# Kernel tuning notes

Hardware: AMD Instinct MI355X
Metric: run time of the kernel (lower is better)

The kernel has to match this reference:

```python
import jax, jax.numpy as jnp
import numpy as np

N_NODES = 100000
N_EDGES = 1600000
IN_CH, HID_CH, OUT_CH, NCLASS = 128, 256, 256, 40


def gcn_conv(x, edge_index, edge_weight, W, b):
    """PyG GCNConv: h = D^{-1/2} (A + I) D^{-1/2} (x @ W) + b, weighted edges."""
    n = x.shape[0]
    row, col = edge_index[0], edge_index[1]
    loop = jnp.arange(n)
    row = jnp.concatenate([row, loop])
    col = jnp.concatenate([col, loop])
    ew = jnp.concatenate([edge_weight, jnp.ones((n,), x.dtype)])  # self-loop weight 1
    deg = jax.ops.segment_sum(ew, col, num_segments=n)
    dinv = jnp.where(deg > 0, jax.lax.rsqrt(deg), 0.0)
    norm = dinv[row] * ew * dinv[col]            # [E+N]
    h = x @ W                                    # transform before propagate (as PyG)
    msg = h[row] * norm[:, None]                 # gather + scale, [E+N, F]
    out = jax.ops.segment_sum(msg, col, num_segments=n)  # scatter-add
    return out + b


def setup_inputs() -> dict:
    key = jax.random.key(0)
    ks = jax.random.split(key, 9)
    x = jax.random.normal(ks[0], (N_NODES, IN_CH), dtype=jnp.float32)
    edge_index = jax.random.randint(ks[1], (2, N_EDGES), 0, N_NODES, dtype=jnp.int64)
    edge_attr = jax.random.uniform(ks[2], (N_EDGES,), dtype=jnp.float32)
    s1 = 1.0 / np.sqrt(IN_CH)
    s2 = 1.0 / np.sqrt(HID_CH)
    s3 = 1.0 / np.sqrt(OUT_CH)
    W1 = jax.random.uniform(ks[3], (IN_CH, HID_CH), jnp.float32, -s1, s1)
    b1 = jnp.zeros((HID_CH,), jnp.float32)
    W2 = jax.random.uniform(ks[4], (HID_CH, OUT_CH), jnp.float32, -s2, s2)
    b2 = jnp.zeros((OUT_CH,), jnp.float32)
    fcW = jax.random.uniform(ks[5], (OUT_CH, NCLASS), jnp.float32, -s3, s3)
    fcb = jax.random.uniform(ks[6], (NCLASS,), jnp.float32, -s3, s3)
    return {"x": x, "edge_index": edge_index, "edge_attr": edge_attr,
            "W1": W1, "b1": b1, "W2": W2, "b2": b2, "fcW": fcW, "fcb": fcb}


def reference(x, edge_index, edge_attr, W1, b1, W2, b2, fcW, fcb):
    # eval mode: dropout is identity
    h = jax.nn.relu(gcn_conv(x, edge_index, edge_attr, W1, b1))
    h = jax.nn.relu(gcn_conv(h, edge_index, edge_attr, W2, b2))
    return h @ fcW + fcb
```

## Files before the change

kernel.cpp:

```cpp
#include <hip/hip_runtime.h>

#define NODES 100000
#define EDGES 1600000

typedef __attribute__((ext_vector_type(8))) short short8;
typedef __attribute__((ext_vector_type(4))) float floatx4;
typedef _Float16 h16;
typedef __attribute__((ext_vector_type(2))) _Float16 h16x2;
typedef __attribute__((ext_vector_type(4))) _Float16 h16x4;
typedef __attribute__((ext_vector_type(8))) _Float16 h16x8;

__device__ inline unsigned short bf16_rne(float x) {
    unsigned u = __float_as_uint(x);
    u += 0x7FFF + ((u >> 16) & 1);
    return (unsigned short)(u >> 16);
}

__device__ inline void load_lds16(void* lds, const void* g) {
    __builtin_amdgcn_global_load_lds((const __attribute__((address_space(1))) void*)g,
                                     (__attribute__((address_space(3))) void*)lds, 16, 0, 0);
}

__global__ __launch_bounds__(256) void k_prep(const float* __restrict__ W1,
                                              unsigned short* __restrict__ W1th, unsigned short* __restrict__ W1tl,
                                              const float* __restrict__ W2,
                                              unsigned short* __restrict__ W2th, unsigned short* __restrict__ W2tl,
                                              const float* __restrict__ x, h16* __restrict__ x16,
                                              unsigned long long* __restrict__ packed, int n) {
    int b = blockIdx.x;
    if (b < 384) {
        const float* W = (b < 128) ? W1 : W2;
        unsigned short* Bth = (b < 128) ? W1th : W2th;
        unsigned short* Btl = (b < 128) ? W1tl : W2tl;
        int K = (b < 128) ? 128 : 256;
        int idx = ((b < 128) ? b : (b - 128)) * 256 + threadIdx.x;
        if (idx < K * 256) {
            int k = idx >> 8, nn = idx & 255;
            float v = W[idx];
            unsigned short h = bf16_rne(v);
            unsigned short l = bf16_rne(v - __uint_as_float((unsigned)h << 16));
            Bth[nn * K + k] = h;
            Btl[nn * K + k] = l;
        }
    } else if (b < 775) {
        int i = (b - 384) * 256 + threadIdx.x;
        if (i < n) packed[i] = 0ull;
    } else {
        int i = (b - 775) * 256 + threadIdx.x;
        if (i < n * 32) {
            float4 v = reinterpret_cast<const float4*>(x)[i];
            h16x4 h;
            h.x = (h16)v.x; h.y = (h16)v.y; h.z = (h16)v.z; h.w = (h16)v.w;
            reinterpret_cast<h16x4*>(x16)[i] = h;
        }
    }
}

__global__ __launch_bounds__(256) void k_hist(unsigned long long* __restrict__ packed,
                                              unsigned short* __restrict__ rank,
                                              const int* __restrict__ col,
                                              const float* __restrict__ ew, int e) {
    int i = blockIdx.x * 256 + threadIdx.x;
    if (i < e) {
        int c = col[i];
        unsigned long long v = (1ull << 40) |
            (unsigned long long)__float2uint_rn(ew[i] * 1048576.0f);
        unsigned long long old = atomicAdd(&packed[c], v);
        rank[i] = (unsigned short)(old >> 40);
    }
}

__global__ __launch_bounds__(256) void k_scan1(const unsigned long long* __restrict__ packed,
                                               int* __restrict__ rowptr,
                                               int* __restrict__ partials,
                                               float* __restrict__ dinv, int n) {
    __shared__ int wtot[4];
    const int tid = threadIdx.x, lane = tid & 63, wid = tid >> 6;
    int i = blockIdx.x * 256 + tid;
    int v = 0;
    if (i < n) {
        unsigned long long p = packed[i];
        v = (int)(p >> 40);
        float deg = 1.0f + (float)(p & 0xFFFFFFFFFFull) * (1.0f / 1048576.0f);
        dinv[i] = rsqrtf(deg);
    }
    int incl = v;
#pragma unroll
    for (int off = 1; off < 64; off <<= 1) {
        int t = __shfl_up(incl, off, 64);
        if (lane >= off) incl += t;
    }
    if (lane == 63) wtot[wid] = incl;
    __syncthreads();
    int woff = 0;
    for (int k = 0; k < wid; ++k) woff += wtot[k];
    if (i < n) rowptr[i] = woff + incl - v;
    if (tid == 255) partials[blockIdx.x] = woff + incl;
}

__global__ __launch_bounds__(512) void k_scan2(int* __restrict__ partials, int nb) {
    __shared__ int wtot[8];
    const int tid = threadIdx.x, lane = tid & 63, wid = tid >> 6;
    int v = (tid < nb) ? partials[tid] : 0;
    int incl = v;
#pragma unroll
    for (int off = 1; off < 64; off <<= 1) {
        int t = __shfl_up(incl, off, 64);
        if (lane >= off) incl += t;
    }
    if (lane == 63) wtot[wid] = incl;
    __syncthreads();
    int woff = 0;
    for (int k = 0; k < wid; ++k) woff += wtot[k];
    if (tid < nb) partials[tid] = woff + incl - v;
}

__global__ __launch_bounds__(256) void k_scan3(int* __restrict__ rowptr,
                                               const int* __restrict__ partials, int n) {
    int i = blockIdx.x * 256 + threadIdx.x;
    if (i < n) rowptr[i] += partials[blockIdx.x];
    if (blockIdx.x == 0 && threadIdx.x == 0) rowptr[n] = EDGES;
}

__global__ __launch_bounds__(256) void k_build(const int* __restrict__ rowptr,
                                               const unsigned short* __restrict__ rank,
                                               int2* __restrict__ meta,
                                               const int* __restrict__ row, const int* __restrict__ col,
                                               const float* __restrict__ ew,
                                               const float* __restrict__ dinv, int e) {
    int i = blockIdx.x * 256 + threadIdx.x;
    if (i >= e) return;
    int r = row[i], c = col[i];
    float w = dinv[r] * ew[i] * dinv[c];
    int pos = rowptr[c] + rank[i];
    meta[pos] = make_int2(r, __float_as_int(w));
}

__global__ __launch_bounds__(256) void k_gather_x(unsigned short* __restrict__ Xh,
                                                  unsigned short* __restrict__ Xl,
                                                  const h16* __restrict__ x16,
                                                  const float* __restrict__ dinv,
                                                  const int* __restrict__ rowptr,
                                                  const int2* __restrict__ meta, int n) {
    int node = (blockIdx.x << 2) + (threadIdx.x >> 6);
    if (node >= n) return;
    const int lane = threadIdx.x & 63;
    const int j = lane << 1;
    float di = dinv[node];
    float s = di * di;
    h16x2 xs = *reinterpret_cast<const h16x2*>(x16 + (size_t)node * 128 + j);
    float2 a0 = make_float2((float)xs.x * s, (float)xs.y * s);
    float2 a1 = make_float2(0.f, 0.f);

    int p = rowptr[node];
    const int end = rowptr[node + 1];
    for (; p + 3 < end; p += 4) {
        int2 m0 = meta[p],     m1 = meta[p + 1];
        int2 m2 = meta[p + 2], m3 = meta[p + 3];
        h16x2 h0 = *reinterpret_cast<const h16x2*>(x16 + (size_t)m0.x * 128 + j);
        h16x2 h1 = *reinterpret_cast<const h16x2*>(x16 + (size_t)m1.x * 128 + j);
        h16x2 h2 = *reinterpret_cast<const h16x2*>(x16 + (size_t)m2.x * 128 + j);
        h16x2 h3 = *reinterpret_cast<const h16x2*>(x16 + (size_t)m3.x * 128 + j);
        float w0 = __int_as_float(m0.y), w1 = __int_as_float(m1.y);
        float w2 = __int_as_float(m2.y), w3 = __int_as_float(m3.y);
        a0.x = fmaf((float)h0.x, w0, a0.x); a0.y = fmaf((float)h0.y, w0, a0.y);
        a1.x = fmaf((float)h1.x, w1, a1.x); a1.y = fmaf((float)h1.y, w1, a1.y);
        a0.x = fmaf((float)h2.x, w2, a0.x); a0.y = fmaf((float)h2.y, w2, a0.y);
        a1.x = fmaf((float)h3.x, w3, a1.x); a1.y = fmaf((float)h3.y, w3, a1.y);
    }
    for (; p < end; ++p) {
        int2 m0 = meta[p];
        h16x2 h0 = *reinterpret_cast<const h16x2*>(x16 + (size_t)m0.x * 128 + j);
        float w0 = __int_as_float(m0.y);
        a0.x = fmaf((float)h0.x, w0, a0.x); a0.y = fmaf((float)h0.y, w0, a0.y);
    }
    a0.x += a1.x; a0.y += a1.y;

    ushort2 hh, ll;
    hh.x = bf16_rne(a0.x); ll.x = bf16_rne(a0.x - __uint_as_float((unsigned)hh.x << 16));
    hh.y = bf16_rne(a0.y); ll.y = bf16_rne(a0.y - __uint_as_float((unsigned)hh.y << 16));
    *reinterpret_cast<ushort2*>(Xh + (size_t)node * 128 + j) = hh;
    *reinterpret_cast<ushort2*>(Xl + (size_t)node * 128 + j) = ll;
}

__global__ __launch_bounds__(256) void k_gather(h16* __restrict__ P,
                                                const h16* __restrict__ H,
                                                const float* __restrict__ dinv,
                                                const int* __restrict__ rowptr,
                                                const int2* __restrict__ meta,
                                                const float* __restrict__ bias, int n) {
    int node = (blockIdx.x << 2) + (threadIdx.x >> 6);
    if (node >= n) return;
    const int lane = threadIdx.x & 63;
    const int j = lane << 2;
    float di = dinv[node];
    float s = di * di;
    float4 b = *reinterpret_cast<const float4*>(bias + j);
    h16x4 hv = *reinterpret_cast<const h16x4*>(H + (size_t)node * 256 + j);
    float4 acc;
    acc.x = fmaf((float)hv.x, s, b.x); acc.y = fmaf((float)hv.y, s, b.y);
    acc.z = fmaf((float)hv.z, s, b.z); acc.w = fmaf((float)hv.w, s, b.w);
    float4 acc2 = make_float4(0.f, 0.f, 0.f, 0.f);

    int p = rowptr[node];
    const int end = rowptr[node + 1];
    for (; p + 3 < end; p += 4) {
        int2 m0 = meta[p],     m1 = meta[p + 1];
        int2 m2 = meta[p + 2], m3 = meta[p + 3];
        h16x4 h0 = *reinterpret_cast<const h16x4*>(H + (size_t)m0.x * 256 + j);
        h16x4 h1 = *reinterpret_cast<const h16x4*>(H + (size_t)m1.x * 256 + j);
        h16x4 h2 = *reinterpret_cast<const h16x4*>(H + (size_t)m2.x * 256 + j);
        h16x4 h3 = *reinterpret_cast<const h16x4*>(H + (size_t)m3.x * 256 + j);
        float w0 = __int_as_float(m0.y), w1 = __int_as_float(m1.y);
        float w2 = __int_as_float(m2.y), w3 = __int_as_float(m3.y);
        acc.x  = fmaf((float)h0.x, w0, acc.x);  acc.y  = fmaf((float)h0.y, w0, acc.y);
        acc.z  = fmaf((float)h0.z, w0, acc.z);  acc.w  = fmaf((float)h0.w, w0, acc.w);
        acc2.x = fmaf((float)h1.x, w1, acc2.x); acc2.y = fmaf((float)h1.y, w1, acc2.y);
        acc2.z = fmaf((float)h1.z, w1, acc2.z); acc2.w = fmaf((float)h1.w, w1, acc2.w);
        acc.x  = fmaf((float)h2.x, w2, acc.x);  acc.y  = fmaf((float)h2.y, w2, acc.y);
        acc.z  = fmaf((float)h2.z, w2, acc.z);  acc.w  = fmaf((float)h2.w, w2, acc.w);
        acc2.x = fmaf((float)h3.x, w3, acc2.x); acc2.y = fmaf((float)h3.y, w3, acc2.y);
        acc2.z = fmaf((float)h3.z, w3, acc2.z); acc2.w = fmaf((float)h3.w, w3, acc2.w);
    }
    for (; p < end; ++p) {
        int2 m0 = meta[p];
        h16x4 h0 = *reinterpret_cast<const h16x4*>(H + (size_t)m0.x * 256 + j);
        float w0 = __int_as_float(m0.y);
        acc.x = fmaf((float)h0.x, w0, acc.x); acc.y = fmaf((float)h0.y, w0, acc.y);
        acc.z = fmaf((float)h0.z, w0, acc.z); acc.w = fmaf((float)h0.w, w0, acc.w);
    }
    acc.x += acc2.x; acc.y += acc2.y; acc.z += acc2.z; acc.w += acc2.w;

    h16x4 o;
    o.x = (h16)fmaxf(acc.x, 0.f); o.y = (h16)fmaxf(acc.y, 0.f);
    o.z = (h16)fmaxf(acc.z, 0.f); o.w = (h16)fmaxf(acc.w, 0.f);
    *reinterpret_cast<h16x4*>(P + (size_t)node * 256 + j) = o;
}

template<bool SPLIT>
__global__ __launch_bounds__(256) void k_gemm_bf16(const unsigned short* __restrict__ Ahg,
                                                   const unsigned short* __restrict__ Alg,
                                                   const unsigned short* __restrict__ Bth,
                                                   const unsigned short* __restrict__ Btl,
                                                   h16* __restrict__ Hh,
                                                   unsigned short* __restrict__ Ph,
                                                   unsigned short* __restrict__ Pl,
                                                   const float* __restrict__ bias,
                                                   int M, int K) {
    __shared__ __attribute__((aligned(16))) char ldsAh[8192];
    __shared__ __attribute__((aligned(16))) char ldsAl[8192];
    __shared__ __attribute__((aligned(16))) char ldsBh[8192];
    __shared__ __attribute__((aligned(16))) char ldsBl[8192];
    const int tid = threadIdx.x;
    const int lane = tid & 63, wid = tid >> 6;
    const int quad = lane >> 4, l16 = lane & 15;
    const int rowBase = blockIdx.x * 128;
    const int colBase = blockIdx.y * 128;
    const int wm = (wid & 1) * 64, wn = (wid >> 1) * 64;

    floatx4 acc[4][4] = {};

    const int c0 = wid * 64 + lane;
    const int c1 = c0 + 256;
    const int r0 = ((c0 >> 6) << 4) + (c0 & 15), q0 = (c0 >> 4) & 3;
    const int r1 = ((c1 >> 6) << 4) + (c1 & 15), q1 = (c1 >> 4) & 3;
    const size_t aoff0 = (size_t)(rowBase + r0) * K + q0 * 8;
    const size_t aoff1 = (size_t)(rowBase + r1) * K + q1 * 8;
    const size_t boff0 = (size_t)(colBase + r0) * K + q0 * 8;
    const size_t boff1 = (size_t)(colBase + r1) * K + q1 * 8;
    const int lo0 = (wid * 64) * 16;
    const int lo1 = (256 + wid * 64) * 16;

    for (int k0 = 0; k0 < K; k0 += 32) {
        load_lds16(ldsAh + lo0, Ahg + aoff0 + k0);
        load_lds16(ldsAh + lo1, Ahg + aoff1 + k0);
        load_lds16(ldsAl + lo0, Alg + aoff0 + k0);
        load_lds16(ldsAl + lo1, Alg + aoff1 + k0);
        load_lds16(ldsBh + lo0, Bth + boff0 + k0);
        load_lds16(ldsBh + lo1, Bth + boff1 + k0);
        load_lds16(ldsBl + lo0, Btl + boff0 + k0);
        load_lds16(ldsBl + lo1, Btl + boff1 + k0);
        __syncthreads();

        const short8* vAh = (const short8*)ldsAh;
        const short8* vAl = (const short8*)ldsAl;
        const short8* vBh = (const short8*)ldsBh;
        const short8* vBl = (const short8*)ldsBl;
        short8 afh[4], afl[4], bfh[4], bfl[4];
#pragma unroll
        for (int mi = 0; mi < 4; ++mi) {
            int idx = ((wm >> 4) + mi) * 64 + quad * 16 + l16;
            afh[mi] = vAh[idx];
            afl[mi] = vAl[idx];
        }
#pragma unroll
        for (int ni = 0; ni < 4; ++ni) {
            int idx = ((wn >> 4) + ni) * 64 + quad * 16 + l16;
            bfh[ni] = vBh[idx];
            bfl[ni] = vBl[idx];
        }
#pragma unroll
        for (int mi = 0; mi < 4; ++mi)
#pragma unroll
            for (int ni = 0; ni < 4; ++ni) {
                acc[mi][ni] = __builtin_amdgcn_mfma_f32_16x16x32_bf16(afh[mi], bfh[ni], acc[mi][ni], 0, 0, 0);
                acc[mi][ni] = __builtin_amdgcn_mfma_f32_16x16x32_bf16(afh[mi], bfl[ni], acc[mi][ni], 0, 0, 0);
                acc[mi][ni] = __builtin_amdgcn_mfma_f32_16x16x32_bf16(afl[mi], bfh[ni], acc[mi][ni], 0, 0, 0);
            }
        __syncthreads();
    }

#pragma unroll
    for (int mi = 0; mi < 4; ++mi) {
#pragma unroll
        for (int r = 0; r < 4; ++r) {
            int grow = rowBase + wm + mi * 16 + quad * 4 + r;
            if (grow < M) {
                if (SPLIT) {
#pragma unroll
                    for (int ni = 0; ni < 4; ++ni) {
                        int gcol = colBase + wn + ni * 16 + l16;
                        float v = acc[mi][ni][r] + bias[gcol];
                        v = fmaxf(v, 0.f);
                        unsigned short h = bf16_rne(v);
                        unsigned short l = bf16_rne(v - __uint_as_float((unsigned)h << 16));
                        Ph[(size_t)grow * 256 + gcol] = h;
                        Pl[(size_t)grow * 256 + gcol] = l;
                    }
                } else {
#pragma unroll
                    for (int ni = 0; ni < 4; ++ni)
                        Hh[(size_t)grow * 256 + colBase + wn + ni * 16 + l16] = (h16)acc[mi][ni][r];
                }
            }
        }
    }
}

__global__ __launch_bounds__(256) void k_fc(float* __restrict__ out, const h16* __restrict__ X,
                                            const float* __restrict__ W, const float* __restrict__ bias,
                                            int M) {
    __shared__ float Ws[256 * 40];
    __shared__ float Xs[32][69];
    const int tid = threadIdx.x;
#pragma unroll
    for (int t = 0; t < 10; ++t) {
        int idx = (t * 256 + tid) * 4;
        *reinterpret_cast<float4*>(&Ws[idx]) = *reinterpret_cast<const float4*>(W + idx);
    }
    const int rowBase = blockIdx.x * 64;
    const int r  = tid >> 2;
    const int cg = (tid & 3) * 10;
    const int kq = (tid & 3) << 3;
    float acc[10] = {};

    for (int k0 = 0; k0 < 256; k0 += 32) {
        int rr = rowBase + r;
        h16x8 v = {};
        if (rr < M) v = *reinterpret_cast<const h16x8*>(X + (size_t)rr * 256 + k0 + kq);
#pragma unroll
        for (int j = 0; j < 8; ++j) Xs[kq + j][r] = (float)v[j];
        __syncthreads();
#pragma unroll
        for (int kk = 0; kk < 32; ++kk) {
            float xv = Xs[kk][r];
#pragma unroll
            for (int j = 0; j < 10; ++j)
                acc[j] = fmaf(xv, Ws[(k0 + kk) * 40 + cg + j], acc[j]);
        }
        __syncthreads();
    }

    int orow = rowBase + r;
    if (orow < M) {
#pragma unroll
        for (int j = 0; j < 10; ++j)
            out[(size_t)orow * 40 + cg + j] = acc[j] + bias[cg + j];
    }
}

extern "C" void kernel_launch(void* const* d_in, const int* in_sizes, int n_in,
                              void* d_out, int out_size, void* d_ws, size_t ws_size,
                              hipStream_t stream) {
    const float* x   = (const float*)d_in[0];
    const int*   ei  = (const int*)d_in[1];
    const float* ea  = (const float*)d_in[2];
    const float* W1  = (const float*)d_in[3];
    const float* b1  = (const float*)d_in[4];
    const float* W2  = (const float*)d_in[5];
    const float* b2  = (const float*)d_in[6];
    const float* fcW = (const float*)d_in[7];
    const float* fcb = (const float*)d_in[8];
    float* out = (float*)d_out;

    const int n = NODES, e = EDGES;
    const int* row = ei;
    const int* col = ei + e;

    char* ws = (char*)d_ws;
    char*  Areg   = ws;
    char*  Breg   = ws + 102400000u;
    float* dinv   = (float*)(ws + 204800000u);
    unsigned long long* packed = (unsigned long long*)(ws + 205200000u);
    int*   rowptr = (int*)  (ws + 206000000u);
    int2*  meta   = (int2*) (ws + 206400016u);
    unsigned short* W1th = (unsigned short*)(ws + 219200016u);
    unsigned short* W1tl = (unsigned short*)(ws + 219265552u);
    unsigned short* W2th = (unsigned short*)(ws + 219331088u);
    unsigned short* W2tl = (unsigned short*)(ws + 219462160u);

    int* partials = (int*)Areg;
    unsigned short* Xah = (unsigned short*)Areg;
    unsigned short* Xal = (unsigned short*)(Areg + 25600000u);
    h16* x16 = (h16*)(Areg + 51200000u);
    h16* H2h = (h16*)Areg;
    unsigned short* rank = (unsigned short*)Breg;
    unsigned short* Ph = (unsigned short*)Breg;
    unsigned short* Pl = (unsigned short*)(Breg + 51200000u);
    h16* P2h = (h16*)Breg;

    const int nb = (n + 255) / 256;
    const int eb = e / 256;

    k_prep<<<13275, 256, 0, stream>>>(W1, W1th, W1tl, W2, W2th, W2tl, x, x16, packed, n);
    k_hist<<<eb, 256, 0, stream>>>(packed, rank, col, ea, e);
    k_scan1<<<nb, 256, 0, stream>>>(packed, rowptr, partials, dinv, n);
    k_scan2<<<1, 512, 0, stream>>>(partials, nb);
    k_scan3<<<nb, 256, 0, stream>>>(rowptr, partials, n);
    k_build<<<eb, 256, 0, stream>>>(rowptr, rank, meta, row, col, ea, dinv, e);

    dim3 gg((n + 127) / 128, 2);

    k_gather_x<<<(n + 3) / 4, 256, 0, stream>>>(Xah, Xal, x16, dinv, rowptr, meta, n);
    k_gemm_bf16<true><<<gg, 256, 0, stream>>>(Xah, Xal, W1th, W1tl, nullptr, Ph, Pl, b1, n, 128);

    k_gemm_bf16<false><<<gg, 256, 0, stream>>>(Ph, Pl, W2th, W2tl, H2h, nullptr, nullptr, nullptr, n, 256);
    k_gather<<<(n + 3) / 4, 256, 0, stream>>>(P2h, H2h, dinv, rowptr, meta, b2, n);

    k_fc<<<(n + 63) / 64, 256, 0, stream>>>(out, P2h, fcW, fcb, n);
}
```

Before: 650.6 us.

## Switch GEMMs from split-bf16 to fp16 activations with split-fp16 weights

Replaces the three-MFMA split-bf16 GEMM with an fp16 scheme. Activations are stored as a single fp16 array and weights are pre-scaled by 64 and split into fp16 hi/lo parts, so each tile needs two MFMAs instead of three. This also halves the activation traffic between the gather and GEMM stages. The weight split and x conversion are folded into the histogram kernel launch, with a small separate init kernel zeroing the counters. In exchange, activations lose precision and could overflow fp16 range.

```diff
diff --git a/kernel.cpp b/kernel.cpp
--- a/kernel.cpp
+++ b/kernel.cpp
@@ -3,70 +3,64 @@
 #define NODES 100000
 #define EDGES 1600000
 
-typedef __attribute__((ext_vector_type(8))) short short8;
 typedef __attribute__((ext_vector_type(4))) float floatx4;
 typedef _Float16 h16;
 typedef __attribute__((ext_vector_type(2))) _Float16 h16x2;
 typedef __attribute__((ext_vector_type(4))) _Float16 h16x4;
 typedef __attribute__((ext_vector_type(8))) _Float16 h16x8;
-
-__device__ inline unsigned short bf16_rne(float x) {
-    unsigned u = __float_as_uint(x);
-    u += 0x7FFF + ((u >> 16) & 1);
-    return (unsigned short)(u >> 16);
-}
+typedef __attribute__((ext_vector_type(8))) _Float16 half8;
+
+#define WSCALE 64.0f
+#define WINV   (1.0f / 64.0f)
 
 __device__ inline void load_lds16(void* lds, const void* g) {
     __builtin_amdgcn_global_load_lds((const __attribute__((address_space(1))) void*)g,
                                      (__attribute__((address_space(3))) void*)lds, 16, 0, 0);
 }
 
-__global__ __launch_bounds__(256) void k_prep(const float* __restrict__ W1,
-                                              unsigned short* __restrict__ W1th, unsigned short* __restrict__ W1tl,
-                                              const float* __restrict__ W2,
-                                              unsigned short* __restrict__ W2th, unsigned short* __restrict__ W2tl,
-                                              const float* __restrict__ x, h16* __restrict__ x16,
-                                              unsigned long long* __restrict__ packed, int n) {
+__global__ __launch_bounds__(256) void k_init(unsigned long long* __restrict__ packed, int n) {
+    int i = blockIdx.x * 256 + threadIdx.x;
+    if (i < n) packed[i] = 0ull;
+}
+
+__device__ inline void w_split(const float* W, h16* Wh, h16* Wl, int idx, int K) {
+    int k = idx >> 8, nn = idx & 255;
+    float v = W[idx] * WSCALE;
+    h16 h = (h16)v;
+    h16 l = (h16)(v - (float)h);
+    Wh[nn * K + k] = h;
+    Wl[nn * K + k] = l;
+}
+
+__global__ __launch_bounds__(256) void k_hist(unsigned long long* __restrict__ packed,
+                                              unsigned short* __restrict__ rank,
+                                              const int* __restrict__ col,
+                                              const float* __restrict__ ew, int e,
+                                              const float* __restrict__ W1, h16* __restrict__ W1h, h16* __restrict__ W1l,
+                                              const float* __restrict__ W2, h16* __restrict__ W2h, h16* __restrict__ W2l,
+                                              const float* __restrict__ x, h16* __restrict__ x16, int n) {
     int b = blockIdx.x;
-    if (b < 384) {
-        const float* W = (b < 128) ? W1 : W2;
-        unsigned short* Bth = (b < 128) ? W1th : W2th;
-        unsigned short* Btl = (b < 128) ? W1tl : W2tl;
-        int K = (b < 128) ? 128 : 256;
-        int idx = ((b < 128) ? b : (b - 128)) * 256 + threadIdx.x;
-        if (idx < K * 256) {
-            int k = idx >> 8, nn = idx & 255;
-            float v = W[idx];
-            unsigned short h = bf16_rne(v);
-            unsigned short l = bf16_rne(v - __uint_as_float((unsigned)h << 16));
-            Bth[nn * K + k] = h;
-            Btl[nn * K + k] = l;
+    if (b < 6250) {
+        int i = b * 256 + threadIdx.x;
+        if (i < e) {
+            int c = col[i];
+            unsigned long long v = (1ull << 40) |
+                (unsigned long long)__float2uint_rn(ew[i] * 1048576.0f);
+            unsigned long long old = atomicAdd(&packed[c], v);
+            rank[i] = (unsigned short)(old >> 40);
         }
-    } else if (b < 775) {
-        int i = (b - 384) * 256 + threadIdx.x;
-        if (i < n) packed[i] = 0ull;
+    } else if (b < 6378) {
+        w_split(W1, W1h, W1l, (b - 6250) * 256 + threadIdx.x, 128);
+    } else if (b < 6634) {
+        w_split(W2, W2h, W2l, (b - 6378) * 256 + threadIdx.x, 256);
     } else {
-        int i = (b - 775) * 256 + threadIdx.x;
+        int i = (b - 6634) * 256 + threadIdx.x;
         if (i < n * 32) {
             float4 v = reinterpret_cast<const float4*>(x)[i];
             h16x4 h;
             h.x = (h16)v.x; h.y = (h16)v.y; h.z = (h16)v.z; h.w = (h16)v.w;
             reinterpret_cast<h16x4*>(x16)[i] = h;
         }
-    }
-}
-
-__global__ __launch_bounds__(256) void k_hist(unsigned long long* __restrict__ packed,
-                                              unsigned short* __restrict__ rank,
-                                              const int* __restrict__ col,
-                                              const float* __restrict__ ew, int e) {
-    int i = blockIdx.x * 256 + threadIdx.x;
-    if (i < e) {
-        int c = col[i];
-        unsigned long long v = (1ull << 40) |
-            (unsigned long long)__float2uint_rn(ew[i] * 1048576.0f);
-        unsigned long long old = atomicAdd(&packed[c], v);
-        rank[i] = (unsigned short)(old >> 40);
     }
 }
 
@@ -136,8 +130,7 @@
     meta[pos] = make_int2(r, __float_as_int(w));
 }
 
-__global__ __launch_bounds__(256) void k_gather_x(unsigned short* __restrict__ Xh,
-                                                  unsigned short* __restrict__ Xl,
+__global__ __launch_bounds__(256) void k_gather_x(h16* __restrict__ Xa,
                                                   const h16* __restrict__ x16,
                                                   const float* __restrict__ dinv,
                                                   const int* __restrict__ rowptr,
@@ -176,11 +169,9 @@
     }
     a0.x += a1.x; a0.y += a1.y;
 
-    ushort2 hh, ll;
-    hh.x = bf16_rne(a0.x); ll.x = bf16_rne(a0.x - __uint_as_float((unsigned)hh.x << 16));
-    hh.y = bf16_rne(a0.y); ll.y = bf16_rne(a0.y - __uint_as_float((unsigned)hh.y << 16));
-    *reinterpret_cast<ushort2*>(Xh + (size_t)node * 128 + j) = hh;
-    *reinterpret_cast<ushort2*>(Xl + (size_t)node * 128 + j) = ll;
+    h16x2 o;
+    o.x = (h16)a0.x; o.y = (h16)a0.y;
+    *reinterpret_cast<h16x2*>(Xa + (size_t)node * 128 + j) = o;
 }
 
 __global__ __launch_bounds__(256) void k_gather(h16* __restrict__ P,
@@ -238,17 +229,13 @@
 }
 
 template<bool SPLIT>
-__global__ __launch_bounds__(256) void k_gemm_bf16(const unsigned short* __restrict__ Ahg,
-                                                   const unsigned short* __restrict__ Alg,
-                                                   const unsigned short* __restrict__ Bth,
-                                                   const unsigned short* __restrict__ Btl,
-                                                   h16* __restrict__ Hh,
-                                                   unsigned short* __restrict__ Ph,
-                                                   unsigned short* __restrict__ Pl,
-                                                   const float* __restrict__ bias,
-                                                   int M, int K) {
-    __shared__ __attribute__((aligned(16))) char ldsAh[8192];
-    __shared__ __attribute__((aligned(16))) char ldsAl[8192];
+__global__ __launch_bounds__(256) void k_gemm_f16(const h16* __restrict__ Ag,
+                                                  const h16* __restrict__ Bhg,
+                                                  const h16* __restrict__ Blg,
+                                                  h16* __restrict__ Out,
+                                                  const float* __restrict__ bias,
+                                                  int M, int K) {
+    __shared__ __attribute__((aligned(16))) char ldsA[8192];
     __shared__ __attribute__((aligned(16))) char ldsBh[8192];
     __shared__ __attribute__((aligned(16))) char ldsBl[8192];
     const int tid = threadIdx.x;
@@ -272,27 +259,21 @@
     const int lo1 = (256 + wid * 64) * 16;
 
     for (int k0 = 0; k0 < K; k0 += 32) {
-        load_lds16(ldsAh + lo0, Ahg + aoff0 + k0);
-        load_lds16(ldsAh + lo1, Ahg + aoff1 + k0);
-        load_lds16(ldsAl + lo0, Alg + aoff0 + k0);
-        load_lds16(ldsAl + lo1, Alg + aoff1 + k0);
-        load_lds16(ldsBh + lo0, Bth + boff0 + k0);
-        load_lds16(ldsBh + lo1, Bth + boff1 + k0);
-        load_lds16(ldsBl + lo0, Btl + boff0 + k0);
-        load_lds16(ldsBl + lo1, Btl + boff1 + k0);
+        load_lds16(ldsA + lo0, Ag + aoff0 + k0);
+        load_lds16(ldsA + lo1, Ag + aoff1 + k0);
+        load_lds16(ldsBh + lo0, Bhg + boff0 + k0);
+        load_lds16(ldsBh + lo1, Bhg + boff1 + k0);
+        load_lds16(ldsBl + lo0, Blg + boff0 + k0);
+        load_lds16(ldsBl + lo1, Blg + boff1 + k0);
         __syncthreads();
 
-        const short8* vAh = (const short8*)ldsAh;
-        const short8* vAl = (const short8*)ldsAl;
-        const short8* vBh = (const short8*)ldsBh;
-        const short8* vBl = (const short8*)ldsBl;
-        short8 afh[4], afl[4], bfh[4], bfl[4];
-#pragma unroll
-        for (int mi = 0; mi < 4; ++mi) {
-            int idx = ((wm >> 4) + mi) * 64 + quad * 16 + l16;
-            afh[mi] = vAh[idx];
-            afl[mi] = vAl[idx];
-        }
+        const half8* vA  = (const half8*)ldsA;
+        const half8* vBh = (const half8*)ldsBh;
+        const half8* vBl = (const half8*)ldsBl;
+        half8 af[4], bfh[4], bfl[4];
+#pragma unroll
+        for (int mi = 0; mi < 4; ++mi)
+            af[mi] = vA[((wm >> 4) + mi) * 64 + quad * 16 + l16];
 #pragma unroll
         for (int ni = 0; ni < 4; ++ni) {
             int idx = ((wn >> 4) + ni) * 64 + quad * 16 + l16;
@@ -303,9 +284,8 @@
         for (int mi = 0; mi < 4; ++mi)
 #pragma unroll
             for (int ni = 0; ni < 4; ++ni) {
-                acc[mi][ni] = __builtin_amdgcn_mfma_f32_16x16x32_bf16(afh[mi], bfh[ni], acc[mi][ni], 0, 0, 0);
-                acc[mi][ni] = __builtin_amdgcn_mfma_f32_16x16x32_bf16(afh[mi], bfl[ni], acc[mi][ni], 0, 0, 0);
-                acc[mi][ni] = __builtin_amdgcn_mfma_f32_16x16x32_bf16(afl[mi], bfh[ni], acc[mi][ni], 0, 0, 0);
+                acc[mi][ni] = __builtin_amdgcn_mfma_f32_16x16x32_f16(af[mi], bfh[ni], acc[mi][ni], 0, 0, 0);
+                acc[mi][ni] = __builtin_amdgcn_mfma_f32_16x16x32_f16(af[mi], bfl[ni], acc[mi][ni], 0, 0, 0);
             }
         __syncthreads();
     }
@@ -316,21 +296,12 @@
         for (int r = 0; r < 4; ++r) {
             int grow = rowBase + wm + mi * 16 + quad * 4 + r;
             if (grow < M) {
-                if (SPLIT) {
-#pragma unroll
-                    for (int ni = 0; ni < 4; ++ni) {
-                        int gcol = colBase + wn + ni * 16 + l16;
-                        float v = acc[mi][ni][r] + bias[gcol];
-                        v = fmaxf(v, 0.f);
-                        unsigned short h = bf16_rne(v);
-                        unsigned short l = bf16_rne(v - __uint_as_float((unsigned)h << 16));
-                        Ph[(size_t)grow * 256 + gcol] = h;
-                        Pl[(size_t)grow * 256 + gcol] = l;
-                    }
-                } else {
-#pragma unroll
-                    for (int ni = 0; ni < 4; ++ni)
-                        Hh[(size_t)grow * 256 + colBase + wn + ni * 16 + l16] = (h16)acc[mi][ni][r];
+#pragma unroll
+                for (int ni = 0; ni < 4; ++ni) {
+                    int gcol = colBase + wn + ni * 16 + l16;
+                    float v = acc[mi][ni][r] * WINV;
+                    if (SPLIT) v = fmaxf(v + bias[gcol], 0.f);
+                    Out[(size_t)grow * 256 + gcol] = (h16)v;
                 }
             }
         }
@@ -404,26 +375,25 @@
     unsigned long long* packed = (unsigned long long*)(ws + 205200000u);
     int*   rowptr = (int*)  (ws + 206000000u);
     int2*  meta   = (int2*) (ws + 206400016u);
-    unsigned short* W1th = (unsigned short*)(ws + 219200016u);
-    unsigned short* W1tl = (unsigned short*)(ws + 219265552u);
-    unsigned short* W2th = (unsigned short*)(ws + 219331088u);
-    unsigned short* W2tl = (unsigned short*)(ws + 219462160u);
+    h16*   W1h    = (h16*)  (ws + 219200016u);
+    h16*   W1l    = (h16*)  (ws + 219265552u);
+    h16*   W2h    = (h16*)  (ws + 219331088u);
+    h16*   W2l    = (h16*)  (ws + 219462160u);
 
     int* partials = (int*)Areg;
-    unsigned short* Xah = (unsigned short*)Areg;
-    unsigned short* Xal = (unsigned short*)(Areg + 25600000u);
-    h16* x16 = (h16*)(Areg + 51200000u);
-    h16* H2h = (h16*)Areg;
+    h16* Xa16 = (h16*)Areg;
+    h16* x16  = (h16*)(Areg + 25600000u);
+    h16* H2h  = (h16*)Areg;
     unsigned short* rank = (unsigned short*)Breg;
-    unsigned short* Ph = (unsigned short*)Breg;
-    unsigned short* Pl = (unsigned short*)(Breg + 51200000u);
-    h16* P2h = (h16*)Breg;
+    h16* P1   = (h16*)Breg;
+    h16* P2h  = (h16*)(Breg + 51200000u);
 
     const int nb = (n + 255) / 256;
     const int eb = e / 256;
 
-    k_prep<<<13275, 256, 0, stream>>>(W1, W1th, W1tl, W2, W2th, W2tl, x, x16, packed, n);
-    k_hist<<<eb, 256, 0, stream>>>(packed, rank, col, ea, e);
+    k_init<<<nb, 256, 0, stream>>>(packed, n);
+    k_hist<<<19134, 256, 0, stream>>>(packed, rank, col, ea, e,
+                                      W1, W1h, W1l, W2, W2h, W2l, x, x16, n);
     k_scan1<<<nb, 256, 0, stream>>>(packed, rowptr, partials, dinv, n);
     k_scan2<<<1, 512, 0, stream>>>(partials, nb);
     k_scan3<<<nb, 256, 0, stream>>>(rowptr, partials, n);
@@ -431,10 +401,10 @@
 
     dim3 gg((n + 127) / 128, 2);
 
-    k_gather_x<<<(n + 3) / 4, 256, 0, stream>>>(Xah, Xal, x16, dinv, rowptr, meta, n);
-    k_gemm_bf16<true><<<gg, 256, 0, stream>>>(Xah, Xal, W1th, W1tl, nullptr, Ph, Pl, b1, n, 128);
-
-    k_gemm_bf16<false><<<gg, 256, 0, stream>>>(Ph, Pl, W2th, W2tl, H2h, nullptr, nullptr, nullptr, n, 256);
+    k_gather_x<<<(n + 3) / 4, 256, 0, stream>>>(Xa16, x16, dinv, rowptr, meta, n);
+    k_gemm_f16<true><<<gg, 256, 0, stream>>>(Xa16, W1h, W1l, P1, b1, n, 128);
+
+    k_gemm_f16<false><<<gg, 256, 0, stream>>>(P1, W2h, W2l, H2h, nullptr, n, 256);
     k_gather<<<(n + 3) / 4, 256, 0, stream>>>(P2h, H2h, dinv, rowptr, meta, b2, n);
 
     k_fc<<<(n + 63) / 64, 256, 0, stream>>>(out, P2h, fcW, fcb, n);
```

Measured after the change: 614.5 us. 5.5% less time.
